# Kernel optimization log

Hardware: AMD Instinct MI355X
Metric: run time of the kernel (lower is better)

The kernel has to match this reference:

```python
import jax, jax.numpy as jnp
import numpy as np

N_NODES = 100000


def gcn_conv(x, W, b, src, dst, n):
    # PyG GCNConv: linear transform, add self-loops, symmetric deg^{-1/2} norm, scatter-sum.
    h = x @ W  # [N, out]
    loop = jnp.arange(n, dtype=src.dtype)
    s = jnp.concatenate([src, loop])
    d = jnp.concatenate([dst, loop])
    deg = jax.ops.segment_sum(jnp.ones_like(d, dtype=h.dtype), d, num_segments=n)
    dinv = jnp.where(deg > 0, jax.lax.rsqrt(deg), 0.0)
    norm = dinv[s] * dinv[d]  # [E+N]
    msg = h[s] * norm[:, None]  # gather + scale
    out = jax.ops.segment_sum(msg, d, num_segments=n)  # scatter-add
    return out + b


def setup_inputs() -> dict:
    key = jax.random.key(0)
    ks = jax.random.split(key, 6)
    in_dim, hid, out_dim = 128, 128, 32
    n_edges = 1600000
    x = jax.random.normal(ks[0], (N_NODES, in_dim), dtype=jnp.float32)
    edge_index = jax.random.randint(ks[1], (2, n_edges), 0, N_NODES, dtype=jnp.int64)
    W1 = jax.random.normal(ks[2], (in_dim, hid), dtype=jnp.float32) / np.sqrt(in_dim)
    b1 = jnp.zeros((hid,), dtype=jnp.float32)
    W2 = jax.random.normal(ks[3], (hid, out_dim), dtype=jnp.float32) / np.sqrt(hid)
    b2 = jnp.zeros((out_dim,), dtype=jnp.float32)
    return {"x": x, "edge_index": edge_index, "W1": W1, "b1": b1, "W2": W2, "b2": b2}


def reference(x, edge_index, W1, b1, W2, b2):
    src, dst = edge_index[0], edge_index[1]
    h = gcn_conv(x, W1, b1, src, dst, N_NODES)
    h = jax.nn.relu(h)
    # F.dropout(training=False) in eval -> identity
    h = gcn_conv(h, W2, b2, src, dst, N_NODES)
    return jax.nn.log_softmax(h, axis=1)
```

## Files before the change

### kernel.cpp

```cpp
#include <hip/hip_runtime.h>
#include <hip/hip_bf16.h>
#include <math.h>

#define N_NODES 100000
#define N_EDGES 1600000
#define NB 196
#define CAP 16000
#define CHUNK 8192

typedef unsigned int uint;
typedef unsigned short ushort_t;
typedef unsigned char uchar_t;
typedef float f32x16 __attribute__((ext_vector_type(16)));
typedef float f32x2 __attribute__((ext_vector_type(2)));
typedef __bf16 bf16x8 __attribute__((ext_vector_type(8)));

__device__ __forceinline__ float bf2f(uint h) {
    union { uint u; float f; } x; x.u = h << 16; return x.f;
}
__device__ __forceinline__ unsigned short f2bf(float f) {
    union { float f; uint u; } x; x.f = f;
    uint u = x.u;
    return (unsigned short)((u + 0x7fffu + ((u >> 16) & 1u)) >> 16);
}
__device__ __forceinline__ uint pk2(float a, float b) {
    return (uint)f2bf(a) | ((uint)f2bf(b) << 16);
}
__device__ __forceinline__ bf16x8 bc8(uint4 u) { return __builtin_bit_cast(bf16x8, u); }

__device__ __forceinline__ int edge_at(const int* __restrict__ ei, int is32, long long idx) {
    return is32 ? ei[idx] : (int)(((const long long*)ei)[idx]);
}

__global__ void k_prep(const float* __restrict__ W1, const float* __restrict__ W2,
                       ushort_t* __restrict__ wt1, ushort_t* __restrict__ w2t,
                       const int* __restrict__ ei, int* __restrict__ flag,
                       int* __restrict__ cnt) {
    int t = threadIdx.x;
    if (blockIdx.x == 0) {
        if (t == 0) *flag = 0;
        if (t < NB) cnt[t] = 0;
        __syncthreads();
        int v = ei[2 * t + 1] | ei[2 * (t + 256) + 1];
        if (v) atomicOr(flag, 1);
    }
    int i = blockIdx.x * 256 + t;
    if (i < 16384) {
        int c = i >> 7, k = i & 127;
        wt1[i] = f2bf(W1[k * 128 + c]);
    } else if (i < 20480) {
        int j = i - 16384;
        int c = j >> 7, p = j & 127;
        int cl = (p & 3) * 32 + (p >> 2);
        w2t[j] = f2bf(W2[cl * 32 + c]);
    }
}


__global__ __launch_bounds__(512) void k_bucket(const int* __restrict__ ei,
                                                const int* __restrict__ flag,
                                                int* __restrict__ cnt,
                                                uint* __restrict__ buf) {
    __shared__ uint stage[CHUNK];
    __shared__ unsigned char bid[CHUNK];
    __shared__ int lcnt[512], ls[256], lbase[256], gbase[256];
    int t = threadIdx.x;
    int is32 = *flag;
    lcnt[t] = 0;
    __syncthreads();
    int base = blockIdx.x * CHUNK;
    int sub = t & 256;
    int srcv[16], dstv[16], offv[16];
    #pragma unroll
    for (int i = 0; i < 16; i++) {
        int e = base + i * 512 + t;
        if (e < N_EDGES) {
            srcv[i] = edge_at(ei, is32, e);
            dstv[i] = edge_at(ei, is32, (long long)N_EDGES + e);
            offv[i] = atomicAdd(&lcnt[sub + (dstv[i] >> 9)], 1);
        } else {
            offv[i] = -1;
        }
    }
    __syncthreads();
    int c = 0;
    if (t < 256) { c = lcnt[t] + lcnt[256 + t]; ls[t] = c; }
    __syncthreads();
    int val = c;
    for (int off = 1; off < 256; off <<= 1) {
        int tmp = (t >= off && t < 256) ? ls[t - off] : 0;
        __syncthreads();
        if (t < 256) { val += tmp; ls[t] = val; }
        __syncthreads();
    }
    if (t < 256) {
        lbase[t] = val - c;
        gbase[t] = (c > 0) ? atomicAdd(&cnt[t], c) : 0;
    }
    __syncthreads();
    int total = ls[255];
    #pragma unroll
    for (int i = 0; i < 16; i++) {
        if (offv[i] >= 0) {
            int b = dstv[i] >> 9;
            int p = lbase[b] + (sub ? lcnt[b] : 0) + offv[i];
            stage[p] = (uint)srcv[i] | ((uint)(dstv[i] & 511) << 17);
            bid[p] = (unsigned char)b;
        }
    }
    __syncthreads();
    for (int idx = t; idx < total; idx += 512) {
        int b = bid[idx];
        int r = gbase[b] + (idx - lbase[b]);
        if (r < CAP) buf[(size_t)b * CAP + r] = stage[idx];
    }
}

__global__ __launch_bounds__(256) void k_build(const uint* __restrict__ buf,
                                               const int* __restrict__ cnt,
                                               int* __restrict__ row_start,
                                               float* __restrict__ dinv,
                                               int* __restrict__ csr_src) {
    __shared__ int ldeg[512], lexc[512], lcur[512], s[256];
    int t = threadIdx.x;
    int b = blockIdx.x;
    int cv = (t < NB) ? cnt[t] : 0;
    s[t] = cv;
    __syncthreads();
    int val = cv;
    for (int off = 1; off < 256; off <<= 1) {
        int tmp = (t >= off) ? s[t - off] : 0;
        __syncthreads();
        val += tmp;
        s[t] = val;
        __syncthreads();
    }
    int obase = (b == 0) ? 0 : s[b - 1];
    if (b == 0 && t == 0) row_start[N_NODES] = N_EDGES;
    int n0 = b << 9;
    int nn = min(512, N_NODES - n0);
    int ne = min(cnt[b], CAP);
    const uint* __restrict__ in = buf + (size_t)b * CAP;
    ldeg[t] = 0; ldeg[t + 256] = 0;
    lcur[t] = 0; lcur[t + 256] = 0;
    __syncthreads();
    for (int idx = t; idx < ne; idx += 256) {
        atomicAdd(&ldeg[in[idx] >> 17], 1);
    }
    __syncthreads();
    int v = ldeg[2 * t] + ldeg[2 * t + 1];
    s[t] = v;
    __syncthreads();
    int val2 = v;
    for (int off = 1; off < 256; off <<= 1) {
        int tmp = (t >= off) ? s[t - off] : 0;
        __syncthreads();
        val2 += tmp;
        s[t] = val2;
        __syncthreads();
    }
    int excl = val2 - v;
    lexc[2 * t] = excl;
    lexc[2 * t + 1] = excl + ldeg[2 * t];
    __syncthreads();
    for (int i = t; i < nn; i += 256) {
        row_start[n0 + i] = obase + lexc[i];
        dinv[n0 + i] = rsqrtf((float)(ldeg[i] + 1));
    }
    __syncthreads();
    for (int idx = t; idx < ne; idx += 256) {
        uint p = in[idx];
        int dl = p >> 17;
        int pos = obase + lexc[dl] + atomicAdd(&lcur[dl], 1);
        csr_src[pos] = (int)(p & 0x1FFFFu);
    }
}

__global__ __launch_bounds__(256) void k_gemm1(const float4* __restrict__ xf,
                                               const uint4* __restrict__ wt1,
                                               const float* __restrict__ dinv,
                                               uint* __restrict__ g1p) {
    __shared__ uint4 WT[128 * 16];
    int t = threadIdx.x;
    #pragma unroll
    for (int i = 0; i < 8; i++) {
        int gi = i * 256 + t;
        int c = gi >> 4, g = gi & 15;
        WT[c * 16 + (g ^ (c & 15))] = wt1[gi];
    }
    __syncthreads();
    int w = t >> 6, l = t & 63;
    int row0 = blockIdx.x * 128 + w * 32;
    int crow = min(row0 + (l & 31), N_NODES - 1);
    int hi = l >> 5;
    f32x16 acc[4];
    #pragma unroll
    for (int ct = 0; ct < 4; ct++)
        #pragma unroll
        for (int r = 0; r < 16; r++) acc[ct][r] = 0.0f;
    const float4* ap = xf + (size_t)crow * 32;
    #pragma unroll
    for (int k0 = 0; k0 < 8; k0++) {
        float4 f0 = ap[(k0 * 2 + hi) * 2];
        float4 f1 = ap[(k0 * 2 + hi) * 2 + 1];
        uint4 au;
        au.x = pk2(f0.x, f0.y); au.y = pk2(f0.z, f0.w);
        au.z = pk2(f1.x, f1.y); au.w = pk2(f1.z, f1.w);
        bf16x8 a = bc8(au);
        #pragma unroll
        for (int ct = 0; ct < 4; ct++) {
            int col = ct * 32 + (l & 31);
            bf16x8 b = bc8(WT[col * 16 + ((k0 * 2 + hi) ^ (col & 15))]);
            acc[ct] = __builtin_amdgcn_mfma_f32_32x32x16_bf16(a, b, acc[ct], 0, 0, 0);
        }
    }
    #pragma unroll
    for (int reg = 0; reg < 16; reg++) {
        int row = row0 + (reg & 3) + 8 * (reg >> 2) + 4 * hi;
        if (row < N_NODES) {
            float d = dinv[row];
            int pw = __builtin_amdgcn_cvt_pk_fp8_f32(acc[0][reg] * d, acc[1][reg] * d, 0, false);
            pw = __builtin_amdgcn_cvt_pk_fp8_f32(acc[2][reg] * d, acc[3][reg] * d, pw, true);
            g1p[(size_t)row * 32 + (l & 31)] = (uint)pw;
        }
    }
}

__global__ __launch_bounds__(256) void k_agg1(const uint4* __restrict__ g1p4,
                                              const float* __restrict__ dinv,
                                              const float* __restrict__ b1,
                                              const int* __restrict__ row_start,
                                              const int* __restrict__ csr_src,
                                              uint4* __restrict__ a1) {
    int v = blockIdx.x * 32 + (threadIdx.x >> 3);
    int a = threadIdx.x & 7;
    float s[4][4];
    {
        uint4 u = g1p4[(size_t)v * 8 + a];
        #pragma unroll
        for (int k = 0; k < 4; k++) {
            uint w = k == 0 ? u.x : k == 1 ? u.y : k == 2 ? u.z : u.w;
            f32x2 lo = __builtin_amdgcn_cvt_pk_f32_fp8(w, false);
            f32x2 hh = __builtin_amdgcn_cvt_pk_f32_fp8(w, true);
            s[k][0] = lo[0]; s[k][1] = lo[1]; s[k][2] = hh[0]; s[k][3] = hh[1];
        }
    }
    int jb = row_start[v], je = row_start[v + 1];
    int j = jb;
    for (; j + 8 <= je; j += 8) {
        int idx[8];
        #pragma unroll
        for (int q = 0; q < 8; q++) idx[q] = csr_src[j + q];
        uint4 d[8];
        #pragma unroll
        for (int q = 0; q < 8; q++) d[q] = g1p4[(size_t)idx[q] * 8 + a];
        #pragma unroll
        for (int q = 0; q < 8; q++) {
            #pragma unroll
            for (int k = 0; k < 4; k++) {
                uint w = k == 0 ? d[q].x : k == 1 ? d[q].y : k == 2 ? d[q].z : d[q].w;
                f32x2 lo = __builtin_amdgcn_cvt_pk_f32_fp8(w, false);
                f32x2 hh = __builtin_amdgcn_cvt_pk_f32_fp8(w, true);
                s[k][0] += lo[0]; s[k][1] += lo[1]; s[k][2] += hh[0]; s[k][3] += hh[1];
            }
        }
    }
    for (; j + 4 <= je; j += 4) {
        int idx[4];
        #pragma unroll
        for (int q = 0; q < 4; q++) idx[q] = csr_src[j + q];
        uint4 d[4];
        #pragma unroll
        for (int q = 0; q < 4; q++) d[q] = g1p4[(size_t)idx[q] * 8 + a];
        #pragma unroll
        for (int q = 0; q < 4; q++) {
            #pragma unroll
            for (int k = 0; k < 4; k++) {
                uint w = k == 0 ? d[q].x : k == 1 ? d[q].y : k == 2 ? d[q].z : d[q].w;
                f32x2 lo = __builtin_amdgcn_cvt_pk_f32_fp8(w, false);
                f32x2 hh = __builtin_amdgcn_cvt_pk_f32_fp8(w, true);
                s[k][0] += lo[0]; s[k][1] += lo[1]; s[k][2] += hh[0]; s[k][3] += hh[1];
            }
        }
    }
    for (; j < je; j++) {
        uint4 u = g1p4[(size_t)csr_src[j] * 8 + a];
        #pragma unroll
        for (int k = 0; k < 4; k++) {
            uint w = k == 0 ? u.x : k == 1 ? u.y : k == 2 ? u.z : u.w;
            f32x2 lo = __builtin_amdgcn_cvt_pk_f32_fp8(w, false);
            f32x2 hh = __builtin_amdgcn_cvt_pk_f32_fp8(w, true);
            s[k][0] += lo[0]; s[k][1] += lo[1]; s[k][2] += hh[0]; s[k][3] += hh[1];
        }
    }
    float dv = dinv[v];
    float o[4][4];
    #pragma unroll
    for (int k = 0; k < 4; k++) {
        int c0 = 4 * a + k;
        o[k][0] = fmaxf(dv * s[k][0] + b1[c0], 0.0f);
        o[k][1] = fmaxf(dv * s[k][1] + b1[32 + c0], 0.0f);
        o[k][2] = fmaxf(dv * s[k][2] + b1[64 + c0], 0.0f);
        o[k][3] = fmaxf(dv * s[k][3] + b1[96 + c0], 0.0f);
    }
    uint4 w0, w1;
    w0.x = pk2(o[0][0], o[0][1]); w0.y = pk2(o[0][2], o[0][3]);
    w0.z = pk2(o[1][0], o[1][1]); w0.w = pk2(o[1][2], o[1][3]);
    w1.x = pk2(o[2][0], o[2][1]); w1.y = pk2(o[2][2], o[2][3]);
    w1.z = pk2(o[3][0], o[3][1]); w1.w = pk2(o[3][2], o[3][3]);
    a1[(size_t)v * 16 + 2 * a]     = w0;
    a1[(size_t)v * 16 + 2 * a + 1] = w1;
}

__global__ __launch_bounds__(256) void k_gemm2(const uint4* __restrict__ a1v,
                                               const uint4* __restrict__ w2t,
                                               const float* __restrict__ dinv,
                                               uchar_t* __restrict__ g2p) {
    __shared__ uint4 WT[32 * 16];
    int t = threadIdx.x;
    #pragma unroll
    for (int i = 0; i < 2; i++) {
        int gi = i * 256 + t;
        int c = gi >> 4, g = gi & 15;
        WT[c * 16 + (g ^ (c & 15))] = w2t[gi];
    }
    __syncthreads();
    int w = t >> 6, l = t & 63;
    int row0 = blockIdx.x * 128 + w * 32;
    int crow = min(row0 + (l & 31), N_NODES - 1);
    int hi = l >> 5;
    int col = l & 31;
    f32x16 acc;
    #pragma unroll
    for (int r = 0; r < 16; r++) acc[r] = 0.0f;
    const uint4* ap = a1v + (size_t)crow * 16;
    #pragma unroll
    for (int k0 = 0; k0 < 8; k0++) {
        bf16x8 a = bc8(ap[k0 * 2 + hi]);
        bf16x8 b = bc8(WT[col * 16 + ((k0 * 2 + hi) ^ (col & 15))]);
        acc = __builtin_amdgcn_mfma_f32_32x32x16_bf16(a, b, acc, 0, 0, 0);
    }
    #pragma unroll
    for (int reg = 0; reg < 16; reg++) {
        int row = row0 + (reg & 3) + 8 * (reg >> 2) + 4 * hi;
        if (row < N_NODES) {
            float z = acc[reg] * dinv[row];
            int pw = __builtin_amdgcn_cvt_pk_fp8_f32(z, z, 0, false);
            g2p[(size_t)row * 32 + col] = (uchar_t)(pw & 0xff);
        }
    }
}

__global__ __launch_bounds__(256) void k_agg2(const uint* __restrict__ g2p4,
                                              const float* __restrict__ dinv,
                                              const float* __restrict__ b2,
                                              const int* __restrict__ row_start,
                                              const int* __restrict__ csr_src,
                                              float4* __restrict__ out) {
    int v = blockIdx.x * 32 + (threadIdx.x >> 3);
    int L = threadIdx.x & 7;
    float s0, s1, s2, s3;
    {
        uint u = g2p4[(size_t)v * 8 + L];
        f32x2 a0 = __builtin_amdgcn_cvt_pk_f32_fp8(u, false);
        f32x2 a1f = __builtin_amdgcn_cvt_pk_f32_fp8(u, true);
        s0 = a0[0]; s1 = a0[1]; s2 = a1f[0]; s3 = a1f[1];
    }
    int jb = row_start[v], je = row_start[v + 1];
    int j = jb;
    for (; j + 8 <= je; j += 8) {
        int i0 = csr_src[j + 0], i1 = csr_src[j + 1];
        int i2 = csr_src[j + 2], i3 = csr_src[j + 3];
        int i4 = csr_src[j + 4], i5 = csr_src[j + 5];
        int i6 = csr_src[j + 6], i7 = csr_src[j + 7];
        uint d0 = g2p4[(size_t)i0 * 8 + L];
        uint d1 = g2p4[(size_t)i1 * 8 + L];
        uint d2 = g2p4[(size_t)i2 * 8 + L];
        uint d3 = g2p4[(size_t)i3 * 8 + L];
        uint d4 = g2p4[(size_t)i4 * 8 + L];
        uint d5 = g2p4[(size_t)i5 * 8 + L];
        uint d6 = g2p4[(size_t)i6 * 8 + L];
        uint d7 = g2p4[(size_t)i7 * 8 + L];
        #pragma unroll
        for (int q = 0; q < 8; q++) {
            uint uu = q == 0 ? d0 : q == 1 ? d1 : q == 2 ? d2 : q == 3 ? d3
                    : q == 4 ? d4 : q == 5 ? d5 : q == 6 ? d6 : d7;
            f32x2 a0 = __builtin_amdgcn_cvt_pk_f32_fp8(uu, false);
            f32x2 a1f = __builtin_amdgcn_cvt_pk_f32_fp8(uu, true);
            s0 += a0[0]; s1 += a0[1]; s2 += a1f[0]; s3 += a1f[1];
        }
    }
    for (; j < je; j++) {
        uint u = g2p4[(size_t)csr_src[j] * 8 + L];
        f32x2 a0 = __builtin_amdgcn_cvt_pk_f32_fp8(u, false);
        f32x2 a1f = __builtin_amdgcn_cvt_pk_f32_fp8(u, true);
        s0 += a0[0]; s1 += a0[1]; s2 += a1f[0]; s3 += a1f[1];
    }
    float dv = dinv[v];
    int c0 = 4 * L;
    float z0 = dv * s0 + b2[c0];
    float z1 = dv * s1 + b2[c0 + 1];
    float z2 = dv * s2 + b2[c0 + 2];
    float z3 = dv * s3 + b2[c0 + 3];
    float m = fmaxf(fmaxf(z0, z1), fmaxf(z2, z3));
    #pragma unroll
    for (int off = 4; off >= 1; off >>= 1) m = fmaxf(m, __shfl_xor(m, off));
    float e = __expf(z0 - m) + __expf(z1 - m) + __expf(z2 - m) + __expf(z3 - m);
    #pragma unroll
    for (int off = 4; off >= 1; off >>= 1) e += __shfl_xor(e, off);
    float lg = __logf(e);
    float4 o;
    o.x = (z0 - m) - lg;
    o.y = (z1 - m) - lg;
    o.z = (z2 - m) - lg;
    o.w = (z3 - m) - lg;
    out[(size_t)v * 8 + L] = o;
}


extern "C" void kernel_launch(void* const* d_in, const int* in_sizes, int n_in,
                              void* d_out, int out_size, void* d_ws, size_t ws_size,
                              hipStream_t stream) {
    const float* x  = (const float*)d_in[0];
    const int*   ei = (const int*)d_in[1];
    const float* W1 = (const float*)d_in[2];
    const float* b1 = (const float*)d_in[3];
    const float* W2 = (const float*)d_in[4];
    const float* b2 = (const float*)d_in[5];
    float* out = (float*)d_out;

    char* ws = (char*)d_ws;
    size_t off = 0;
    auto alloc = [&](size_t bytes) {
        void* p = ws + off;
        off = (off + bytes + 255) & ~255ULL;
        return p;
    };
    int* flag = (int*)alloc(4);
    int* cnt  = (int*)alloc((size_t)NB * 4);
    int*   row_start = (int*)alloc((size_t)(N_NODES + 1) * 4);
    float* dinv      = (float*)alloc((size_t)N_NODES * 4);
    int*   csr_src   = (int*)alloc((size_t)N_EDGES * 4);
    ushort_t* wt1g   = (ushort_t*)alloc(16384 * 2);
    ushort_t* w2tg   = (ushort_t*)alloc(4096 * 2);
    uint*  g1p       = (uint*)alloc((size_t)N_NODES * 128);
    void* uregion = alloc((size_t)N_NODES * 128 * 2);
    uint*  buf = (uint*)uregion;
    uint4* a1  = (uint4*)uregion;
    uchar_t* g2p = (uchar_t*)g1p;

    k_prep<<<80, 256, 0, stream>>>(W1, W2, wt1g, w2tg, ei, flag, cnt);
    k_bucket<<<(N_EDGES + CHUNK - 1) / CHUNK, 512, 0, stream>>>(ei, flag, cnt, buf);
    k_build<<<NB, 256, 0, stream>>>(buf, cnt, row_start, dinv, csr_src);
    k_gemm1<<<(N_NODES + 127) / 128, 256, 0, stream>>>((const float4*)x, (const uint4*)wt1g, dinv, g1p);
    k_agg1<<<N_NODES / 32, 256, 0, stream>>>((const uint4*)g1p, dinv, b1, row_start, csr_src, a1);
    k_gemm2<<<(N_NODES + 127) / 128, 256, 0, stream>>>((const uint4*)a1, (const uint4*)w2tg, dinv, g2p);
    k_agg2<<<N_NODES / 32, 256, 0, stream>>>((const uint*)g2p, dinv, b2, row_start, csr_src, (float4*)out);
}
```

Measured before the change: 137.5 us.

## Halve destination bucket width to double CSR-build blocks and split degree atomics

Edges are bucketed by dst>>8 instead of dst>>9, which doubles the bucket count (391) and halves the per-bucket capacity and the bucket-kernel chunk size. The build kernel then launches twice as many blocks, each handling 256 nodes with one node per thread, and spreads the degree histogram over two sub-arrays to reduce LDS atomic contention. The intent is more parallelism and less serialization in the CSR construction. In exchange, the bucket kernel runs more blocks with a wider 512-entry scan and issues more global atomics, and the obase prefix now combines pairs of counts.

Result: faster. 130.9 us (-4.8%).

```diff
diff --git a/kernel.cpp b/kernel.cpp
--- a/kernel.cpp
+++ b/kernel.cpp
@@ -4,9 +4,9 @@
 
 #define N_NODES 100000
 #define N_EDGES 1600000
-#define NB 196
-#define CAP 16000
-#define CHUNK 8192
+#define NB 391
+#define CAP 6000
+#define CHUNK 4096
 
 typedef unsigned int uint;
 typedef unsigned short ushort_t;
@@ -40,6 +40,7 @@
     if (blockIdx.x == 0) {
         if (t == 0) *flag = 0;
         if (t < NB) cnt[t] = 0;
+        if (t + 256 < NB) cnt[t + 256] = 0;
         __syncthreads();
         int v = ei[2 * t + 1] | ei[2 * (t + 256) + 1];
         if (v) atomicOr(flag, 1);
@@ -62,50 +63,50 @@
                                                 int* __restrict__ cnt,
                                                 uint* __restrict__ buf) {
     __shared__ uint stage[CHUNK];
-    __shared__ unsigned char bid[CHUNK];
-    __shared__ int lcnt[512], ls[256], lbase[256], gbase[256];
+    __shared__ ushort_t bid[CHUNK];
+    __shared__ int lcnt[1024];
+    __shared__ int ls[512], lbase[512], gbase[512];
     int t = threadIdx.x;
     int is32 = *flag;
-    lcnt[t] = 0;
+    lcnt[t] = 0; lcnt[t + 512] = 0;
     __syncthreads();
     int base = blockIdx.x * CHUNK;
-    int sub = t & 256;
-    int srcv[16], dstv[16], offv[16];
-    #pragma unroll
-    for (int i = 0; i < 16; i++) {
+    int sub = (t & 256) << 1;
+    int srcv[8], dstv[8], offv[8];
+    #pragma unroll
+    for (int i = 0; i < 8; i++) {
         int e = base + i * 512 + t;
         if (e < N_EDGES) {
             srcv[i] = edge_at(ei, is32, e);
             dstv[i] = edge_at(ei, is32, (long long)N_EDGES + e);
-            offv[i] = atomicAdd(&lcnt[sub + (dstv[i] >> 9)], 1);
+            offv[i] = atomicAdd(&lcnt[sub + (dstv[i] >> 8)], 1);
         } else {
             offv[i] = -1;
         }
     }
     __syncthreads();
-    int c = 0;
-    if (t < 256) { c = lcnt[t] + lcnt[256 + t]; ls[t] = c; }
+    int c = lcnt[t] + lcnt[512 + t];
+    ls[t] = c;
     __syncthreads();
     int val = c;
-    for (int off = 1; off < 256; off <<= 1) {
-        int tmp = (t >= off && t < 256) ? ls[t - off] : 0;
-        __syncthreads();
-        if (t < 256) { val += tmp; ls[t] = val; }
-        __syncthreads();
-    }
-    if (t < 256) {
-        lbase[t] = val - c;
-        gbase[t] = (c > 0) ? atomicAdd(&cnt[t], c) : 0;
-    }
-    __syncthreads();
-    int total = ls[255];
-    #pragma unroll
-    for (int i = 0; i < 16; i++) {
+    for (int off = 1; off < 512; off <<= 1) {
+        int tmp = (t >= off) ? ls[t - off] : 0;
+        __syncthreads();
+        val += tmp;
+        ls[t] = val;
+        __syncthreads();
+    }
+    lbase[t] = val - c;
+    gbase[t] = (c > 0) ? atomicAdd(&cnt[t], c) : 0;
+    __syncthreads();
+    int total = ls[511];
+    #pragma unroll
+    for (int i = 0; i < 8; i++) {
         if (offv[i] >= 0) {
-            int b = dstv[i] >> 9;
+            int b = dstv[i] >> 8;
             int p = lbase[b] + (sub ? lcnt[b] : 0) + offv[i];
-            stage[p] = (uint)srcv[i] | ((uint)(dstv[i] & 511) << 17);
-            bid[p] = (unsigned char)b;
+            stage[p] = (uint)srcv[i] | ((uint)(dstv[i] & 255) << 17);
+            bid[p] = (ushort_t)b;
         }
     }
     __syncthreads();
@@ -121,13 +122,14 @@
                                                int* __restrict__ row_start,
                                                float* __restrict__ dinv,
                                                int* __restrict__ csr_src) {
-    __shared__ int ldeg[512], lexc[512], lcur[512], s[256];
+    __shared__ int ldeg[512], lexc[256], lcur[256], s[256];
     int t = threadIdx.x;
     int b = blockIdx.x;
-    int cv = (t < NB) ? cnt[t] : 0;
-    s[t] = cv;
-    __syncthreads();
-    int val = cv;
+    int i2 = 2 * t;
+    int cv2 = ((i2 < NB) ? cnt[i2] : 0) + ((i2 + 1 < NB) ? cnt[i2 + 1] : 0);
+    s[t] = cv2;
+    __syncthreads();
+    int val = cv2;
     for (int off = 1; off < 256; off <<= 1) {
         int tmp = (t >= off) ? s[t - off] : 0;
         __syncthreads();
@@ -135,23 +137,24 @@
         s[t] = val;
         __syncthreads();
     }
-    int obase = (b == 0) ? 0 : s[b - 1];
+    int obase = ((b >> 1) ? s[(b >> 1) - 1] : 0) + ((b & 1) ? cnt[b - 1] : 0);
     if (b == 0 && t == 0) row_start[N_NODES] = N_EDGES;
-    int n0 = b << 9;
-    int nn = min(512, N_NODES - n0);
+    int n0 = b << 8;
+    int nn = min(256, N_NODES - n0);
     int ne = min(cnt[b], CAP);
     const uint* __restrict__ in = buf + (size_t)b * CAP;
     ldeg[t] = 0; ldeg[t + 256] = 0;
-    lcur[t] = 0; lcur[t + 256] = 0;
-    __syncthreads();
+    lcur[t] = 0;
+    __syncthreads();
+    int sub = (t & 128) << 1;
     for (int idx = t; idx < ne; idx += 256) {
-        atomicAdd(&ldeg[in[idx] >> 17], 1);
-    }
-    __syncthreads();
-    int v = ldeg[2 * t] + ldeg[2 * t + 1];
-    s[t] = v;
-    __syncthreads();
-    int val2 = v;
+        atomicAdd(&ldeg[sub + (in[idx] >> 17)], 1);
+    }
+    __syncthreads();
+    int dv = ldeg[t] + ldeg[256 + t];
+    s[t] = dv;
+    __syncthreads();
+    int val2 = dv;
     for (int off = 1; off < 256; off <<= 1) {
         int tmp = (t >= off) ? s[t - off] : 0;
         __syncthreads();
@@ -159,13 +162,11 @@
         s[t] = val2;
         __syncthreads();
     }
-    int excl = val2 - v;
-    lexc[2 * t] = excl;
-    lexc[2 * t + 1] = excl + ldeg[2 * t];
-    __syncthreads();
-    for (int i = t; i < nn; i += 256) {
-        row_start[n0 + i] = obase + lexc[i];
-        dinv[n0 + i] = rsqrtf((float)(ldeg[i] + 1));
+    int excl = val2 - dv;
+    lexc[t] = excl;
+    if (t < nn) {
+        row_start[n0 + t] = obase + excl;
+        dinv[n0 + t] = rsqrtf((float)(dv + 1));
     }
     __syncthreads();
     for (int idx = t; idx < ne; idx += 256) {
```
